# Kernel tuning notes

Measured on AMD Instinct MI355X. Metric: run time of the kernel, lower is better.

Reference implementation:

```python
import jax, jax.numpy as jnp
import numpy as np

B, T, C = 8, 2048, 1024
DK = 64  # d_k = n_embd // n_head = 1024 // 16


def setup_inputs() -> dict:
    key = jax.random.key(0)
    ks = jax.random.split(key, 4)
    X = jax.random.normal(ks[0], (B, T, C), dtype=jnp.float32)
    scale = 1.0 / np.sqrt(C)
    Wq = jax.random.normal(ks[1], (C, DK), dtype=jnp.float32) * scale
    Wk = jax.random.normal(ks[2], (C, DK), dtype=jnp.float32) * scale
    Wv = jax.random.normal(ks[3], (C, DK), dtype=jnp.float32) * scale
    bq = jnp.zeros((DK,), dtype=jnp.float32)
    bk = jnp.zeros((DK,), dtype=jnp.float32)
    bv = jnp.zeros((DK,), dtype=jnp.float32)
    return {"X": X, "Wq": Wq, "bq": bq, "Wk": Wk, "bk": bk, "Wv": Wv, "bv": bv}


def reference(X, Wq, bq, Wk, bk, Wv, bv):
    # Single-head causal self-attention (dropout disabled / eval mode).
    T_ = X.shape[1]
    Q = X @ Wq + bq  # [B, T, d_k]
    K = X @ Wk + bk
    V = X @ Wv + bv
    scores = jnp.einsum('btd,bsd->bts', Q, K) / jnp.sqrt(jnp.float32(Q.shape[-1]))
    causal = jnp.tril(jnp.ones((T_, T_), dtype=bool))  # tril mask
    scores = jnp.where(causal, scores, -jnp.inf)
    weights = jax.nn.softmax(scores, axis=-1)
    out = jnp.einsum('bts,bsd->btd', weights, V)  # [B, T, d_k]
    return out
```

## Files before the change

kernel.cpp:

```cpp
#include <hip/hip_runtime.h>
#include <math.h>

#define NB 8
#define NT 2048
#define NC 1024
#define DK 64
#define BT (NB*NT)

#define QKV_BYTES  (3u * BT * DK * 2u)
#define SLOT_BYTES 8704u

typedef unsigned short ushort_t;
typedef unsigned int uint_t;
typedef __attribute__((ext_vector_type(8))) short short8;
typedef __attribute__((ext_vector_type(4))) float f32x4;

__device__ __forceinline__ float bf2f(uint_t u) {
    union { uint_t i; float f; } v;
    v.i = u << 16;
    return v.f;
}
__device__ __forceinline__ ushort_t f2bf(float f) {
    union { float f; uint_t i; } v; v.f = f;
    uint_t x = v.i;
    return (ushort_t)((x + 0x7fffu + ((x >> 16) & 1u)) >> 16);
}
__device__ __forceinline__ uint_t pack2bf(float lo, float hi) {
    return (uint_t)f2bf(lo) | ((uint_t)f2bf(hi) << 16);
}

__device__ __forceinline__ int seg_prefix(int qt) {
    const int a = qt >> 2;
    return 2 * a * (a + 1) - 4 + (qt & 3) * (a + 1);
}

__global__ __launch_bounds__(256) void wt_prep_kernel(
    const float* __restrict__ Wq, const float* __restrict__ Wk,
    const float* __restrict__ Wv, ushort_t* __restrict__ WtG)
{
    const int tg = blockIdx.x * 256 + threadIdx.x;
    const int n  = tg >> 7;
    const int k0 = (tg & 127) * 8;
    const float* W = (n < 64) ? Wq : (n < 128) ? Wk : Wv;
    const int nc = n & 63;
    ushort_t o[8];
    #pragma unroll
    for (int j = 0; j < 8; ++j) o[j] = f2bf(W[(size_t)(k0 + j) * DK + nc]);
    *reinterpret_cast<uint4*>(&WtG[n * NC + k0]) = *reinterpret_cast<uint4*>(o);
}

__global__ __launch_bounds__(512, 4) void qkv_mfma_kernel(
    const float* __restrict__ X, const ushort_t* __restrict__ WtG,
    const float* __restrict__ bq, const float* __restrict__ bk,
    const float* __restrict__ bv, ushort_t* __restrict__ QKV)
{
    __shared__ ushort_t Xs[2][2][32 * 72];
    __shared__ float    Racc[32 * 196];
    __shared__ ushort_t VtL[64 * 40];

    const int t    = threadIdx.x;
    const int grp  = t >> 8;
    const int tg   = t & 255;
    const int w    = (t >> 6) & 3;
    const int lane = t & 63;
    const int g    = lane >> 4;
    const int col  = lane & 15;
    const int m0   = blockIdx.x * 32;
    const int kb   = grp * 512;

    const int xrow = tg >> 3;
    const int xc   = (tg & 7) * 8;

    float xf[8];
    short8 wA[6], wB[6];

    auto LOADX = [&](int k0) {
        const float4* xp = reinterpret_cast<const float4*>(
            &X[(size_t)(m0 + xrow) * NC + kb + k0 + xc]);
        float4 v0 = xp[0], v1 = xp[1];
        xf[0] = v0.x; xf[1] = v0.y; xf[2] = v0.z; xf[3] = v0.w;
        xf[4] = v1.x; xf[5] = v1.y; xf[6] = v1.z; xf[7] = v1.w;
    };
    auto LOADW = [&](int k0, short8* wn) {
        #pragma unroll
        for (int tj = 0; tj < 3; ++tj) {
            const int ng = 48 * w + 16 * tj + col;
            #pragma unroll
            for (int c = 0; c < 2; ++c)
                wn[tj * 2 + c] = *reinterpret_cast<const short8*>(
                    &WtG[ng * NC + kb + k0 + 32 * c + 8 * g]);
        }
    };
    auto WRITEX = [&](int b) {
        ushort_t xb[8];
        #pragma unroll
        for (int j = 0; j < 8; ++j) xb[j] = f2bf(xf[j]);
        *reinterpret_cast<uint4*>(&Xs[grp][b][xrow * 72 + xc]) =
            *reinterpret_cast<uint4*>(xb);
    };

    f32x4 acc[2][3];
    #pragma unroll
    for (int ri = 0; ri < 2; ++ri)
        #pragma unroll
        for (int tj = 0; tj < 3; ++tj) acc[ri][tj] = (f32x4){0.f, 0.f, 0.f, 0.f};

    auto COMPUTE = [&](int cur, short8* wc) {
        const ushort_t* XsB = Xs[grp][cur];
        #pragma unroll
        for (int c = 0; c < 2; ++c) {
            short8 af[2];
            #pragma unroll
            for (int ri = 0; ri < 2; ++ri)
                af[ri] = *reinterpret_cast<const short8*>(
                    &XsB[(16 * ri + col) * 72 + 32 * c + 8 * g]);
            #pragma unroll
            for (int ri = 0; ri < 2; ++ri)
                #pragma unroll
                for (int tj = 0; tj < 3; ++tj)
                    acc[ri][tj] = __builtin_amdgcn_mfma_f32_16x16x32_bf16(
                        af[ri], wc[tj * 2 + c], acc[ri][tj], 0, 0, 0);
        }
    };

    LOADX(0);
    LOADW(0, wA);
    WRITEX(0);

    #pragma unroll
    for (int ks2 = 0; ks2 < 4; ++ks2) {
        {
            const int ks = 2 * ks2;
            if (ks < 7) { LOADX((ks + 1) * 64); LOADW((ks + 1) * 64, wB); }
            __syncthreads();
            COMPUTE(0, wA);
            if (ks < 7) WRITEX(1);
        }
        {
            const int ks = 2 * ks2 + 1;
            if (ks < 7) { LOADX((ks + 1) * 64); LOADW((ks + 1) * 64, wA); }
            __syncthreads();
            COMPUTE(1, wB);
            if (ks < 7) WRITEX(0);
        }
    }

    __syncthreads();
    if (grp == 1) {
        #pragma unroll
        for (int ri = 0; ri < 2; ++ri)
            #pragma unroll
            for (int tj = 0; tj < 3; ++tj)
                #pragma unroll
                for (int r = 0; r < 4; ++r)
                    Racc[(16 * ri + 4 * g + r) * 196 + 48 * w + 16 * tj + col] =
                        acc[ri][tj][r];
    }
    __syncthreads();
    if (grp == 0) {
        #pragma unroll
        for (int ri = 0; ri < 2; ++ri)
            #pragma unroll
            for (int tj = 0; tj < 3; ++tj)
                #pragma unroll
                for (int r = 0; r < 4; ++r)
                    acc[ri][tj][r] +=
                        Racc[(16 * ri + 4 * g + r) * 196 + 48 * w + 16 * tj + col];

        #pragma unroll
        for (int tj = 0; tj < 3; ++tj) {
            const int ng    = 48 * w + 16 * tj + col;
            const int which = ng >> 6, ncol = ng & 63;
            const float* bp = (which == 0) ? bq : (which == 1) ? bk : bv;
            const float bb  = bp[ncol];
            if (which == 2) {
                #pragma unroll
                for (int ri = 0; ri < 2; ++ri)
                    #pragma unroll
                    for (int r = 0; r < 4; ++r)
                        VtL[ncol * 40 + 16 * ri + 4 * g + r] = f2bf(acc[ri][tj][r] + bb);
            } else {
                const float qs = (which == 0) ? 0.125f : 1.0f;
                ushort_t* Y = QKV + (size_t)which * BT * DK;
                #pragma unroll
                for (int ri = 0; ri < 2; ++ri)
                    #pragma unroll
                    for (int r = 0; r < 4; ++r) {
                        const int rowg = m0 + 16 * ri + 4 * g + r;
                        Y[(size_t)rowg * DK + ncol] = f2bf((acc[ri][tj][r] + bb) * qs);
                    }
            }
        }
    }
    __syncthreads();
    if (grp == 0) {
        ushort_t* Vt = QKV + (size_t)2 * BT * DK;
        const int d  = tg >> 2;
        const int sg = tg & 3;
        uint4 v = *reinterpret_cast<const uint4*>(&VtL[d * 40 + sg * 8]);
        *reinterpret_cast<uint4*>(&Vt[(size_t)d * BT + m0 + sg * 8]) = v;
    }
}

__global__ __launch_bounds__(256) void attn_seg_kernel(
    const ushort_t* __restrict__ QKV, float* __restrict__ Out,
    char* __restrict__ Pbase)
{
    const ushort_t* Qw = QKV;
    const ushort_t* Kw = QKV + (size_t)BT * DK;
    const ushort_t* Vw = QKV + (size_t)2 * BT * DK;

    __shared__ ushort_t Ks[256 * 72];
    __shared__ ushort_t VtL[64 * 288];

    const int t     = threadIdx.x;
    const int w     = t >> 6;
    const int lane  = t & 63;
    const int g     = lane >> 4;
    const int col   = lane & 15;
    const int batch = blockIdx.x & 7;
    const int u     = blockIdx.x >> 3;

    int s;
    if      (u < 16) s = 0;
    else if (u < 30) s = 1;
    else if (u < 42) s = 2;
    else if (u < 52) s = 3;
    else if (u < 60) s = 4;
    else if (u < 66) s = 5;
    else if (u < 70) s = 6;
    else             s = 7;
    const int off2 = 16 * s - s * (s - 1);
    const int qt0  = 4 * s + 2 * (u - off2);
    const int kbase = 256 * s;
    const int ntile = min(4, qt0 + 2 - 4 * s);

    {
        const int sr = t >> 2;
        const int ss = t & 3;
        for (int i = 0; i < ntile; ++i) {
            const int krow = 64 * i + sr;
            const size_t gk = ((size_t)(batch * NT) + kbase + krow) * DK + ss * 16;
            const uint4* kp = reinterpret_cast<const uint4*>(Kw + gk);
            *reinterpret_cast<uint4*>(&Ks[krow * 72 + ss * 16])     = kp[0];
            *reinterpret_cast<uint4*>(&Ks[krow * 72 + ss * 16 + 8]) = kp[1];
            const size_t gv = (size_t)sr * BT + (batch * NT + kbase + 64 * i) + ss * 16;
            const uint4* vp = reinterpret_cast<const uint4*>(Vw + gv);
            *reinterpret_cast<uint4*>(&VtL[sr * 288 + 72 * i + ss * 16])     = vp[0];
            *reinterpret_cast<uint4*>(&VtL[sr * 288 + 72 * i + ss * 16 + 8]) = vp[1];
        }
    }
    __syncthreads();

    #pragma unroll
    for (int iq = 0; iq < 2; ++iq) {
        const int qt   = qt0 + iq;
        const int qrow = qt * 64 + 16 * w + col;
        const int kcnt = min(4, qt - 4 * s + 1);
        const int diag = qt - 4 * s;

        short8 qf0, qf1;
        {
            const ushort_t* Qrow = Qw + ((size_t)(batch * NT) + qrow) * DK;
            qf0 = *reinterpret_cast<const short8*>(Qrow + 8 * g);
            qf1 = *reinterpret_cast<const short8*>(Qrow + 32 + 8 * g);
        }

        f32x4 Oa[4];
        #pragma unroll
        for (int dt = 0; dt < 4; ++dt) Oa[dt] = (f32x4){0.f, 0.f, 0.f, 0.f};
        float m = -INFINITY, l = 0.0f;

        for (int ktl = 0; ktl < kcnt; ++ktl) {
            f32x4 sa[4];
            #pragma unroll
            for (int tj = 0; tj < 4; ++tj) sa[tj] = (f32x4){0.f, 0.f, 0.f, 0.f};
            #pragma unroll
            for (int tj = 0; tj < 4; ++tj) {
                const ushort_t* kb = &Ks[(64 * ktl + col + 16 * tj) * 72 + 8 * g];
                short8 kf0 = *reinterpret_cast<const short8*>(kb);
                short8 kf1 = *reinterpret_cast<const short8*>(kb + 32);
                sa[tj] = __builtin_amdgcn_mfma_f32_16x16x32_bf16(kf0, qf0, sa[tj], 0, 0, 0);
                sa[tj] = __builtin_amdgcn_mfma_f32_16x16x32_bf16(kf1, qf1, sa[tj], 0, 0, 0);
            }

            float sv[4][4];
            #pragma unroll
            for (int tj = 0; tj < 4; ++tj)
                #pragma unroll
                for (int r = 0; r < 4; ++r) sv[tj][r] = sa[tj][r];

            if (ktl == diag) {
                const int s0 = (kbase + 64 * ktl);
                #pragma unroll
                for (int tj = 0; tj < 4; ++tj)
                    #pragma unroll
                    for (int r = 0; r < 4; ++r)
                        if (s0 + 16 * tj + 4 * g + r > qrow) sv[tj][r] = -INFINITY;
            }

            float vmax = sv[0][0];
            #pragma unroll
            for (int tj = 0; tj < 4; ++tj)
                #pragma unroll
                for (int r = 0; r < 4; ++r) vmax = fmaxf(vmax, sv[tj][r]);
            vmax = fmaxf(vmax, __shfl_xor(vmax, 16, 64));
            vmax = fmaxf(vmax, __shfl_xor(vmax, 32, 64));

            const float mn = fmaxf(m, vmax);
            const float sc = __expf(m - mn);
            m = mn;

            float p[4][4];
            float lt = 0.f;
            #pragma unroll
            for (int tj = 0; tj < 4; ++tj)
                #pragma unroll
                for (int r = 0; r < 4; ++r) {
                    p[tj][r] = __expf(sv[tj][r] - mn);
                    lt += p[tj][r];
                }
            lt += __shfl_xor(lt, 16, 64);
            lt += __shfl_xor(lt, 32, 64);
            l = l * sc + lt;

            float sco[4];
            #pragma unroll
            for (int r = 0; r < 4; ++r) sco[r] = __shfl(sc, 20 * g + r, 64);
            #pragma unroll
            for (int dt = 0; dt < 4; ++dt)
                #pragma unroll
                for (int r = 0; r < 4; ++r) Oa[dt][r] *= sco[r];

            uint_t pk0[4], pk1[4];
            #pragma unroll
            for (int tj = 0; tj < 4; ++tj) {
                pk0[tj] = pack2bf(p[tj][0], p[tj][1]);
                pk1[tj] = pack2bf(p[tj][2], p[tj][3]);
            }
            const int sA = col + 32 * (g & 1);
            const int sB = sA + 16;
            const bool hi = (g >= 2);

            #pragma unroll
            for (int c = 0; c < 2; ++c) {
                uint_t w0a = __shfl(pk0[2*c], sA, 64), w0b = __shfl(pk0[2*c+1], sA, 64);
                uint_t w1a = __shfl(pk1[2*c], sA, 64), w1b = __shfl(pk1[2*c+1], sA, 64);
                uint_t w2a = __shfl(pk0[2*c], sB, 64), w2b = __shfl(pk0[2*c+1], sB, 64);
                uint_t w3a = __shfl(pk1[2*c], sB, 64), w3b = __shfl(pk1[2*c+1], sB, 64);
                uint_t pa[4];
                pa[0] = hi ? w0b : w0a;
                pa[1] = hi ? w1b : w1a;
                pa[2] = hi ? w2b : w2a;
                pa[3] = hi ? w3b : w3a;
                short8 paf = *reinterpret_cast<const short8*>(pa);
                #pragma unroll
                for (int dt = 0; dt < 4; ++dt) {
                    short8 vf = *reinterpret_cast<const short8*>(
                        &VtL[(col + 16 * dt) * 288 + 72 * ktl + 32 * c + 8 * g]);
                    Oa[dt] = __builtin_amdgcn_mfma_f32_16x16x32_bf16(paf, vf, Oa[dt], 0, 0, 0);
                }
            }
        }

        float lr[4];
        #pragma unroll
        for (int r = 0; r < 4; ++r) lr[r] = __shfl(l, 20 * g + r, 64);

        if (qt < 4) {
            #pragma unroll
            for (int r = 0; r < 4; ++r) {
                const float inv = 1.0f / lr[r];
                const int row = qt * 64 + 16 * w + 4 * g + r;
                float* op = Out + ((size_t)(batch * NT) + row) * DK + col;
                #pragma unroll
                for (int dt = 0; dt < 4; ++dt) op[16 * dt] = Oa[dt][r] * inv;
            }
        } else {
            float mr[4];
            #pragma unroll
            for (int r = 0; r < 4; ++r) mr[r] = __shfl(m, 20 * g + r, 64);
            const int slot = batch * 140 + seg_prefix(qt) + s;
            char* sp = Pbase + (size_t)slot * SLOT_BYTES;
            ushort_t* Ob  = reinterpret_cast<ushort_t*>(sp);
            float*    Pm  = reinterpret_cast<float*>(sp + 8192);
            float*    Plv = reinterpret_cast<float*>(sp + 8448);
            #pragma unroll
            for (int r = 0; r < 4; ++r) {
                const int rloc = 16 * w + 4 * g + r;
                #pragma unroll
                for (int dt = 0; dt < 4; ++dt)
                    Ob[rloc * 64 + 16 * dt + col] = f2bf(Oa[dt][r]);
                if (col == 0) { Pm[rloc] = mr[r]; Plv[rloc] = lr[r]; }
            }
        }
    }
}

__global__ __launch_bounds__(256) void attn_combine_kernel(
    const char* __restrict__ Pbase, float* __restrict__ Out)
{
    const int bid   = blockIdx.x;
    const int batch = bid / 28;
    const int qt    = 4 + bid % 28;
    const int nseg  = (qt >> 2) + 1;
    const int slot0 = batch * 140 + seg_prefix(qt);

    const int t   = threadIdx.x;
    const int row = t >> 2;
    const int d0  = (t & 3) * 16;

    float ms[8], ls[8];
    float M = -INFINITY;
    #pragma unroll
    for (int s = 0; s < 8; ++s)
        if (s < nseg) {
            const char* sp = Pbase + (size_t)(slot0 + s) * SLOT_BYTES;
            ms[s] = reinterpret_cast<const float*>(sp + 8192)[row];
            ls[s] = reinterpret_cast<const float*>(sp + 8448)[row];
            M = fmaxf(M, ms[s]);
        }

    float acc[16];
    #pragma unroll
    for (int j = 0; j < 16; ++j) acc[j] = 0.f;
    float ltot = 0.f;

    #pragma unroll
    for (int s = 0; s < 8; ++s)
        if (s < nseg) {
            const float wsc = __expf(ms[s] - M);
            ltot += wsc * ls[s];
            const ushort_t* Ob = reinterpret_cast<const ushort_t*>(
                Pbase + (size_t)(slot0 + s) * SLOT_BYTES) + row * 64 + d0;
            uint4 u0 = *reinterpret_cast<const uint4*>(Ob);
            uint4 u1 = *reinterpret_cast<const uint4*>(Ob + 8);
            const uint_t* uu = reinterpret_cast<const uint_t*>(&u0);
            #pragma unroll
            for (int j = 0; j < 4; ++j) {
                acc[2*j+0] += wsc * bf2f(uu[j] & 0xffffu);
                acc[2*j+1] += wsc * bf2f(uu[j] >> 16);
            }
            const uint_t* uv = reinterpret_cast<const uint_t*>(&u1);
            #pragma unroll
            for (int j = 0; j < 4; ++j) {
                acc[8+2*j+0] += wsc * bf2f(uv[j] & 0xffffu);
                acc[8+2*j+1] += wsc * bf2f(uv[j] >> 16);
            }
        }

    const float inv = 1.0f / ltot;
    float* op = Out + ((size_t)(batch * NT) + qt * 64 + row) * DK + d0;
    #pragma unroll
    for (int j = 0; j < 16; ++j) op[j] = acc[j] * inv;
}

extern "C" void kernel_launch(void* const* d_in, const int* in_sizes, int n_in,
                              void* d_out, int out_size, void* d_ws, size_t ws_size,
                              hipStream_t stream) {
    const float* X  = (const float*)d_in[0];
    const float* Wq = (const float*)d_in[1];
    const float* bq = (const float*)d_in[2];
    const float* Wk = (const float*)d_in[3];
    const float* bk = (const float*)d_in[4];
    const float* Wv = (const float*)d_in[5];
    const float* bv = (const float*)d_in[6];
    float* Out = (float*)d_out;
    ushort_t* QKV = (ushort_t*)d_ws;
    char* Pbase   = (char*)d_ws + QKV_BYTES;
    ushort_t* WtG = (ushort_t*)d_out;

    wt_prep_kernel<<<96, 256, 0, stream>>>(Wq, Wk, Wv, WtG);
    qkv_mfma_kernel<<<512, 512, 0, stream>>>(X, WtG, bq, bk, bv, QKV);
    attn_seg_kernel<<<576, 256, 0, stream>>>(QKV, Out, Pbase);
    attn_combine_kernel<<<224, 256, 0, stream>>>(Pbase, Out);
}
```

Measured before the change: 66.12 us.

## Fuse both query tiles into one key loop sharing K/V fragment loads

Merges the two sequential per-query-tile attention loops into a single loop over key tiles. Each K and V LDS fragment is now loaded once and fed to MFMAs for both query tiles. The two independent online-softmax chains are interleaved to expose more instruction-level parallelism. It also raises wave priority with s_setprio around the MFMA blocks. In exchange it roughly doubles accumulator register use, and the first query tile runs one extra fully masked key tile.

```diff
diff --git a/kernel.cpp b/kernel.cpp
--- a/kernel.cpp
+++ b/kernel.cpp
@@ -233,7 +233,8 @@
     const int off2 = 16 * s - s * (s - 1);
     const int qt0  = 4 * s + 2 * (u - off2);
     const int kbase = 256 * s;
-    const int ntile = min(4, qt0 + 2 - 4 * s);
+    const int diag0 = qt0 - 4 * s;
+    const int ntile = min(4, diag0 + 2);
 
     {
         const int sr = t >> 2;
@@ -252,120 +253,169 @@
     }
     __syncthreads();
 
+    const int qrow0 = qt0 * 64 + 16 * w + col;
+    const int qrow1 = qrow0 + 64;
+
+    short8 q0a, q0b, q1a, q1b;
+    {
+        const ushort_t* Qr0 = Qw + ((size_t)(batch * NT) + qrow0) * DK;
+        q0a = *reinterpret_cast<const short8*>(Qr0 + 8 * g);
+        q0b = *reinterpret_cast<const short8*>(Qr0 + 32 + 8 * g);
+        const ushort_t* Qr1 = Qw + ((size_t)(batch * NT) + qrow1) * DK;
+        q1a = *reinterpret_cast<const short8*>(Qr1 + 8 * g);
+        q1b = *reinterpret_cast<const short8*>(Qr1 + 32 + 8 * g);
+    }
+
+    f32x4 Oa0[4], Oa1[4];
+    #pragma unroll
+    for (int dt = 0; dt < 4; ++dt) {
+        Oa0[dt] = (f32x4){0.f, 0.f, 0.f, 0.f};
+        Oa1[dt] = (f32x4){0.f, 0.f, 0.f, 0.f};
+    }
+    float m0 = -INFINITY, l0 = 0.0f;
+    float m1 = -INFINITY, l1 = 0.0f;
+
+    for (int ktl = 0; ktl < ntile; ++ktl) {
+        f32x4 sa0[4], sa1[4];
+        #pragma unroll
+        for (int tj = 0; tj < 4; ++tj) {
+            sa0[tj] = (f32x4){0.f, 0.f, 0.f, 0.f};
+            sa1[tj] = (f32x4){0.f, 0.f, 0.f, 0.f};
+        }
+        __builtin_amdgcn_s_setprio(1);
+        #pragma unroll
+        for (int tj = 0; tj < 4; ++tj) {
+            const ushort_t* kb = &Ks[(64 * ktl + col + 16 * tj) * 72 + 8 * g];
+            short8 kf0 = *reinterpret_cast<const short8*>(kb);
+            short8 kf1 = *reinterpret_cast<const short8*>(kb + 32);
+            sa0[tj] = __builtin_amdgcn_mfma_f32_16x16x32_bf16(kf0, q0a, sa0[tj], 0, 0, 0);
+            sa0[tj] = __builtin_amdgcn_mfma_f32_16x16x32_bf16(kf1, q0b, sa0[tj], 0, 0, 0);
+            sa1[tj] = __builtin_amdgcn_mfma_f32_16x16x32_bf16(kf0, q1a, sa1[tj], 0, 0, 0);
+            sa1[tj] = __builtin_amdgcn_mfma_f32_16x16x32_bf16(kf1, q1b, sa1[tj], 0, 0, 0);
+        }
+        __builtin_amdgcn_s_setprio(0);
+
+        const int s0 = kbase + 64 * ktl;
+        if (ktl >= diag0) {
+            #pragma unroll
+            for (int tj = 0; tj < 4; ++tj)
+                #pragma unroll
+                for (int r = 0; r < 4; ++r)
+                    if (s0 + 16 * tj + 4 * g + r > qrow0) sa0[tj][r] = -INFINITY;
+        }
+        if (ktl >= diag0 + 1) {
+            #pragma unroll
+            for (int tj = 0; tj < 4; ++tj)
+                #pragma unroll
+                for (int r = 0; r < 4; ++r)
+                    if (s0 + 16 * tj + 4 * g + r > qrow1) sa1[tj][r] = -INFINITY;
+        }
+
+        float vx0 = sa0[0][0], vx1 = sa1[0][0];
+        #pragma unroll
+        for (int tj = 0; tj < 4; ++tj)
+            #pragma unroll
+            for (int r = 0; r < 4; ++r) {
+                vx0 = fmaxf(vx0, sa0[tj][r]);
+                vx1 = fmaxf(vx1, sa1[tj][r]);
+            }
+        vx0 = fmaxf(vx0, __shfl_xor(vx0, 16, 64));
+        vx1 = fmaxf(vx1, __shfl_xor(vx1, 16, 64));
+        vx0 = fmaxf(vx0, __shfl_xor(vx0, 32, 64));
+        vx1 = fmaxf(vx1, __shfl_xor(vx1, 32, 64));
+
+        const float mn0 = fmaxf(m0, vx0);
+        const float mn1 = fmaxf(m1, vx1);
+        const float sc0 = __expf(m0 - mn0);
+        const float sc1 = __expf(m1 - mn1);
+        m0 = mn0; m1 = mn1;
+
+        float lt0 = 0.f, lt1 = 0.f;
+        #pragma unroll
+        for (int tj = 0; tj < 4; ++tj)
+            #pragma unroll
+            for (int r = 0; r < 4; ++r) {
+                sa0[tj][r] = __expf(sa0[tj][r] - mn0);
+                sa1[tj][r] = __expf(sa1[tj][r] - mn1);
+                lt0 += sa0[tj][r];
+                lt1 += sa1[tj][r];
+            }
+        lt0 += __shfl_xor(lt0, 16, 64);
+        lt1 += __shfl_xor(lt1, 16, 64);
+        lt0 += __shfl_xor(lt0, 32, 64);
+        lt1 += __shfl_xor(lt1, 32, 64);
+        l0 = l0 * sc0 + lt0;
+        l1 = l1 * sc1 + lt1;
+
+        float sco0[4], sco1[4];
+        #pragma unroll
+        for (int r = 0; r < 4; ++r) {
+            sco0[r] = __shfl(sc0, 20 * g + r, 64);
+            sco1[r] = __shfl(sc1, 20 * g + r, 64);
+        }
+        #pragma unroll
+        for (int dt = 0; dt < 4; ++dt)
+            #pragma unroll
+            for (int r = 0; r < 4; ++r) {
+                Oa0[dt][r] *= sco0[r];
+                Oa1[dt][r] *= sco1[r];
+            }
+
+        uint_t pk00[4], pk01[4], pk10[4], pk11[4];
+        #pragma unroll
+        for (int tj = 0; tj < 4; ++tj) {
+            pk00[tj] = pack2bf(sa0[tj][0], sa0[tj][1]);
+            pk01[tj] = pack2bf(sa0[tj][2], sa0[tj][3]);
+            pk10[tj] = pack2bf(sa1[tj][0], sa1[tj][1]);
+            pk11[tj] = pack2bf(sa1[tj][2], sa1[tj][3]);
+        }
+        const int sA = col + 32 * (g & 1);
+        const int sB = sA + 16;
+        const bool hi = (g >= 2);
+
+        #pragma unroll
+        for (int c = 0; c < 2; ++c) {
+            uint_t a0 = __shfl(pk00[2*c], sA, 64), b0 = __shfl(pk00[2*c+1], sA, 64);
+            uint_t a1 = __shfl(pk01[2*c], sA, 64), b1 = __shfl(pk01[2*c+1], sA, 64);
+            uint_t a2 = __shfl(pk00[2*c], sB, 64), b2 = __shfl(pk00[2*c+1], sB, 64);
+            uint_t a3 = __shfl(pk01[2*c], sB, 64), b3 = __shfl(pk01[2*c+1], sB, 64);
+            uint_t c0 = __shfl(pk10[2*c], sA, 64), d0 = __shfl(pk10[2*c+1], sA, 64);
+            uint_t c1 = __shfl(pk11[2*c], sA, 64), d1 = __shfl(pk11[2*c+1], sA, 64);
+            uint_t c2 = __shfl(pk10[2*c], sB, 64), d2 = __shfl(pk10[2*c+1], sB, 64);
+            uint_t c3 = __shfl(pk11[2*c], sB, 64), d3 = __shfl(pk11[2*c+1], sB, 64);
+            uint_t pa0[4], pa1[4];
+            pa0[0] = hi ? b0 : a0;
+            pa0[1] = hi ? b1 : a1;
+            pa0[2] = hi ? b2 : a2;
+            pa0[3] = hi ? b3 : a3;
+            pa1[0] = hi ? d0 : c0;
+            pa1[1] = hi ? d1 : c1;
+            pa1[2] = hi ? d2 : c2;
+            pa1[3] = hi ? d3 : c3;
+            short8 paf0 = *reinterpret_cast<const short8*>(pa0);
+            short8 paf1 = *reinterpret_cast<const short8*>(pa1);
+            __builtin_amdgcn_s_setprio(1);
+            #pragma unroll
+            for (int dt = 0; dt < 4; ++dt) {
+                short8 vf = *reinterpret_cast<const short8*>(
+                    &VtL[(col + 16 * dt) * 288 + 72 * ktl + 32 * c + 8 * g]);
+                Oa0[dt] = __builtin_amdgcn_mfma_f32_16x16x32_bf16(paf0, vf, Oa0[dt], 0, 0, 0);
+                Oa1[dt] = __builtin_amdgcn_mfma_f32_16x16x32_bf16(paf1, vf, Oa1[dt], 0, 0, 0);
+            }
+            __builtin_amdgcn_s_setprio(0);
+        }
+    }
+
     #pragma unroll
     for (int iq = 0; iq < 2; ++iq) {
-        const int qt   = qt0 + iq;
-        const int qrow = qt * 64 + 16 * w + col;
-        const int kcnt = min(4, qt - 4 * s + 1);
-        const int diag = qt - 4 * s;
-
-        short8 qf0, qf1;
-        {
-            const ushort_t* Qrow = Qw + ((size_t)(batch * NT) + qrow) * DK;
-            qf0 = *reinterpret_cast<const short8*>(Qrow + 8 * g);
-            qf1 = *reinterpret_cast<const short8*>(Qrow + 32 + 8 * g);
-        }
-
-        f32x4 Oa[4];
-        #pragma unroll
-        for (int dt = 0; dt < 4; ++dt) Oa[dt] = (f32x4){0.f, 0.f, 0.f, 0.f};
-        float m = -INFINITY, l = 0.0f;
-
-        for (int ktl = 0; ktl < kcnt; ++ktl) {
-            f32x4 sa[4];
-            #pragma unroll
-            for (int tj = 0; tj < 4; ++tj) sa[tj] = (f32x4){0.f, 0.f, 0.f, 0.f};
-            #pragma unroll
-            for (int tj = 0; tj < 4; ++tj) {
-                const ushort_t* kb = &Ks[(64 * ktl + col + 16 * tj) * 72 + 8 * g];
-                short8 kf0 = *reinterpret_cast<const short8*>(kb);
-                short8 kf1 = *reinterpret_cast<const short8*>(kb + 32);
-                sa[tj] = __builtin_amdgcn_mfma_f32_16x16x32_bf16(kf0, qf0, sa[tj], 0, 0, 0);
-                sa[tj] = __builtin_amdgcn_mfma_f32_16x16x32_bf16(kf1, qf1, sa[tj], 0, 0, 0);
-            }
-
-            float sv[4][4];
-            #pragma unroll
-            for (int tj = 0; tj < 4; ++tj)
-                #pragma unroll
-                for (int r = 0; r < 4; ++r) sv[tj][r] = sa[tj][r];
-
-            if (ktl == diag) {
-                const int s0 = (kbase + 64 * ktl);
-                #pragma unroll
-                for (int tj = 0; tj < 4; ++tj)
-                    #pragma unroll
-                    for (int r = 0; r < 4; ++r)
-                        if (s0 + 16 * tj + 4 * g + r > qrow) sv[tj][r] = -INFINITY;
-            }
-
-            float vmax = sv[0][0];
-            #pragma unroll
-            for (int tj = 0; tj < 4; ++tj)
-                #pragma unroll
-                for (int r = 0; r < 4; ++r) vmax = fmaxf(vmax, sv[tj][r]);
-            vmax = fmaxf(vmax, __shfl_xor(vmax, 16, 64));
-            vmax = fmaxf(vmax, __shfl_xor(vmax, 32, 64));
-
-            const float mn = fmaxf(m, vmax);
-            const float sc = __expf(m - mn);
-            m = mn;
-
-            float p[4][4];
-            float lt = 0.f;
-            #pragma unroll
-            for (int tj = 0; tj < 4; ++tj)
-                #pragma unroll
-                for (int r = 0; r < 4; ++r) {
-                    p[tj][r] = __expf(sv[tj][r] - mn);
-                    lt += p[tj][r];
-                }
-            lt += __shfl_xor(lt, 16, 64);
-            lt += __shfl_xor(lt, 32, 64);
-            l = l * sc + lt;
-
-            float sco[4];
-            #pragma unroll
-            for (int r = 0; r < 4; ++r) sco[r] = __shfl(sc, 20 * g + r, 64);
-            #pragma unroll
-            for (int dt = 0; dt < 4; ++dt)
-                #pragma unroll
-                for (int r = 0; r < 4; ++r) Oa[dt][r] *= sco[r];
-
-            uint_t pk0[4], pk1[4];
-            #pragma unroll
-            for (int tj = 0; tj < 4; ++tj) {
-                pk0[tj] = pack2bf(p[tj][0], p[tj][1]);
-                pk1[tj] = pack2bf(p[tj][2], p[tj][3]);
-            }
-            const int sA = col + 32 * (g & 1);
-            const int sB = sA + 16;
-            const bool hi = (g >= 2);
-
-            #pragma unroll
-            for (int c = 0; c < 2; ++c) {
-                uint_t w0a = __shfl(pk0[2*c], sA, 64), w0b = __shfl(pk0[2*c+1], sA, 64);
-                uint_t w1a = __shfl(pk1[2*c], sA, 64), w1b = __shfl(pk1[2*c+1], sA, 64);
-                uint_t w2a = __shfl(pk0[2*c], sB, 64), w2b = __shfl(pk0[2*c+1], sB, 64);
-                uint_t w3a = __shfl(pk1[2*c], sB, 64), w3b = __shfl(pk1[2*c+1], sB, 64);
-                uint_t pa[4];
-                pa[0] = hi ? w0b : w0a;
-                pa[1] = hi ? w1b : w1a;
-                pa[2] = hi ? w2b : w2a;
-                pa[3] = hi ? w3b : w3a;
-                short8 paf = *reinterpret_cast<const short8*>(pa);
-                #pragma unroll
-                for (int dt = 0; dt < 4; ++dt) {
-                    short8 vf = *reinterpret_cast<const short8*>(
-                        &VtL[(col + 16 * dt) * 288 + 72 * ktl + 32 * c + 8 * g]);
-                    Oa[dt] = __builtin_amdgcn_mfma_f32_16x16x32_bf16(paf, vf, Oa[dt], 0, 0, 0);
-                }
-            }
-        }
+        const int qt = qt0 + iq;
+        const float mm = iq ? m1 : m0;
+        const float ll = iq ? l1 : l0;
+        const f32x4* Oa = iq ? Oa1 : Oa0;
 
         float lr[4];
         #pragma unroll
-        for (int r = 0; r < 4; ++r) lr[r] = __shfl(l, 20 * g + r, 64);
+        for (int r = 0; r < 4; ++r) lr[r] = __shfl(ll, 20 * g + r, 64);
 
         if (qt < 4) {
             #pragma unroll
@@ -379,7 +429,7 @@
         } else {
             float mr[4];
             #pragma unroll
-            for (int r = 0; r < 4; ++r) mr[r] = __shfl(m, 20 * g + r, 64);
+            for (int r = 0; r < 4; ++r) mr[r] = __shfl(mm, 20 * g + r, 64);
             const int slot = batch * 140 + seg_prefix(qt) + s;
             char* sp = Pbase + (size_t)slot * SLOT_BYTES;
             ushort_t* Ob  = reinterpret_cast<ushort_t*>(sp);
```

Result: no change. 66.17 us (+0.1%).
